# Kernel tuning notes

Hardware: AMD Instinct MI355X
Metric: run time of the kernel (lower is better)

## Reference

```python
import jax, jax.numpy as jnp
import numpy as np

DIM = 320
D_STATE = 32
D_CONV = 4
EXPAND = 2
HEADDIM = 80
D_INNER = EXPAND * DIM          # 640
NHEADS = D_INNER // HEADDIM     # 8
NGROUPS = 1
CONV_DIM = D_INNER + 2 * NGROUPS * D_STATE          # 704
D_IN_PROJ = 2 * D_INNER + 2 * NGROUPS * D_STATE + NHEADS  # 1352
PATCH = (16, 16, 16)
NUM_PT_EMB = 2


def setup_inputs() -> dict:
    key = jax.random.key(0)
    ks = jax.random.split(key, 16)
    B, Np = 4, 8
    x = jax.random.normal(ks[0], (B, DIM) + PATCH, dtype=jnp.float32)
    point_coords = jax.random.uniform(ks[1], (B, Np, 3), dtype=jnp.float32) * jnp.asarray(PATCH, jnp.float32)
    point_labels = jax.random.randint(ks[2], (B, Np), 0, 2)
    return {
        "x": x,
        "point_coords": point_coords,
        "ln_w": jnp.ones((DIM,), jnp.float32),
        "ln_b": jnp.zeros((DIM,), jnp.float32),
        "in_proj_w": jax.random.normal(ks[3], (D_IN_PROJ, DIM), jnp.float32) * 0.02,
        "conv_w": jax.random.normal(ks[4], (CONV_DIM, 1, D_CONV), jnp.float32) * 0.2,
        "conv_b": jax.random.normal(ks[5], (CONV_DIM,), jnp.float32) * 0.02,
        "dt_bias": jax.random.uniform(ks[6], (NHEADS,), jnp.float32, 0.0, 0.1),
        "A_log": jnp.log(jax.random.uniform(ks[7], (NHEADS,), jnp.float32, 1.0, 16.0)),
        "Dp": jnp.ones((NHEADS,), jnp.float32),
        "rms_w": jnp.ones((D_INNER,), jnp.float32),
        "out_proj_w": jax.random.normal(ks[8], (DIM, D_INNER), jnp.float32) * 0.02,
        "pe_gauss": jax.random.normal(ks[9], (3, DIM // 2), jnp.float32),
        "point_embed": jax.random.normal(ks[10], (NUM_PT_EMB, DIM), jnp.float32) * 0.02,
        "not_a_point": jax.random.normal(ks[11], (DIM,), jnp.float32) * 0.02,
        "point_labels": point_labels,
    }


def _forward(x, point_coords, ln_w, ln_b, in_proj_w, conv_w, conv_b, dt_bias,
             A_log, Dp, rms_w, out_proj_w, pe_gauss, point_embed, not_a_point,
             point_labels):
    B, C = x.shape[:2]
    img_dims = x.shape[2:]
    n_tokens = int(np.prod(img_dims))
    xf = x.reshape(B, C, n_tokens).transpose(0, 2, 1)  # (B, T, C)

    # ---- PointEncoder (SAM-style random Fourier positional embedding) ----
    pc = point_coords / jnp.asarray(PATCH, x.dtype)     # normalize to [0,1]
    pc = 2.0 * pc - 1.0
    pe = (2.0 * jnp.pi) * (pc @ pe_gauss)               # (B, Np, DIM/2)
    pemb = jnp.concatenate([jnp.sin(pe), jnp.cos(pe)], axis=-1)  # (B, Np, DIM)
    lbl = point_labels[..., None]
    safe = jnp.clip(point_labels, 0, NUM_PT_EMB - 1)
    pemb = jnp.where(lbl == -1, not_a_point, pemb + point_embed[safe])

    seq = jnp.concatenate([xf, pemb], axis=1)           # (B, L, C)
    L = seq.shape[1]

    # ---- LayerNorm ----
    mu = seq.mean(-1, keepdims=True)
    var = jnp.mean((seq - mu) ** 2, axis=-1, keepdims=True)
    xn = (seq - mu) * jax.lax.rsqrt(var + 1e-5) * ln_w + ln_b

    # ---- Mamba2 ----
    zxbcdt = xn @ in_proj_w.T                            # (B, L, 1352)
    z = zxbcdt[..., :D_INNER]
    xBC = zxbcdt[..., D_INNER:D_INNER + CONV_DIM]
    dt = zxbcdt[..., D_INNER + CONV_DIM:]                # (B, L, H)
    dt = jax.nn.softplus(dt + dt_bias)

    # causal depthwise conv1d over channels
    conv = jax.lax.conv_general_dilated(
        xBC.transpose(0, 2, 1), conv_w, (1,), [(D_CONV - 1, 0)],
        feature_group_count=CONV_DIM,
        dimension_numbers=("NCH", "OIH", "NCH"))
    xBC = jax.nn.silu((conv + conv_b[None, :, None]).transpose(0, 2, 1))

    xs = xBC[..., :D_INNER].reshape(B, L, NHEADS, HEADDIM)
    Bm = xBC[..., D_INNER:D_INNER + D_STATE]             # (B, L, N), ngroups=1
    Cm = xBC[..., D_INNER + D_STATE:]                    # (B, L, N)

    A = -jnp.exp(A_log)                                  # (H,)
    dA = jnp.exp(dt * A)                                 # (B, L, H)

    def step(h, inp):
        dA_t, dt_t, B_t, C_t, x_t = inp
        h = h * dA_t[:, :, None, None] + jnp.einsum('bh,bn,bhp->bhpn', dt_t, B_t, x_t)
        y = jnp.einsum('bhpn,bn->bhp', h, C_t)
        return h, y

    inps = (dA.transpose(1, 0, 2), dt.transpose(1, 0, 2),
            Bm.transpose(1, 0, 2), Cm.transpose(1, 0, 2),
            xs.transpose(1, 0, 2, 3))
    h0 = jnp.zeros((B, NHEADS, HEADDIM, D_STATE), x.dtype)
    _, ys = jax.lax.scan(step, h0, inps)                 # (L, B, H, P)
    y = ys.transpose(1, 0, 2, 3) + xs * Dp[None, None, :, None]
    y = y.reshape(B, L, D_INNER)

    # gated RMSNorm
    y = y * jax.nn.silu(z)
    y = y * jax.lax.rsqrt(jnp.mean(y * y, axis=-1, keepdims=True) + 1e-5) * rms_w
    out = y @ out_proj_w.T                               # (B, L, DIM)

    out = out[:, :n_tokens].transpose(0, 2, 1).reshape(B, C, *img_dims)
    return out


def reference(x, point_coords, ln_w, ln_b, in_proj_w, conv_w, conv_b, dt_bias,
              A_log, Dp, rms_w, out_proj_w, pe_gauss, point_embed, not_a_point,
              point_labels):
    return _forward(x, point_coords, ln_w, ln_b, in_proj_w, conv_w, conv_b,
                    dt_bias, A_log, Dp, rms_w, out_proj_w, pe_gauss,
                    point_embed, not_a_point, point_labels)
```

## Files before the change

### kernel.cpp

```cpp
#include <hip/hip_runtime.h>
#include <math.h>

#define BQ 4
#define LQ 4104
#define NTQ 4096
#define CDIM 320
#define DIP 1352
#define DI 640
#define CONVD 704
#define NH 8
#define HD 80
#define DS 32
#define MQ (BQ*LQ)
#define QC 64
#define NC 65

typedef __attribute__((ext_vector_type(8))) short bf16x8;
typedef __attribute__((ext_vector_type(4))) float f32x4;

__device__ __forceinline__ unsigned short f2bf(float f){
  union { float f; unsigned u; } v; v.f = f;
  unsigned r = v.u + 0x7FFFu + ((v.u >> 16) & 1u);
  return (unsigned short)(r >> 16);
}
__device__ __forceinline__ float bf2f(unsigned short u){
  union { unsigned u; float f; } v; v.u = ((unsigned)u) << 16;
  return v.f;
}
__device__ __forceinline__ float warp_sum(float v){
  #pragma unroll
  for (int o = 32; o; o >>= 1) v += __shfl_xor(v, o);
  return v;
}
__device__ __forceinline__ void gload16(const unsigned short* g, unsigned short* l){
  __builtin_amdgcn_global_load_lds(
      (const __attribute__((address_space(1))) unsigned int*)g,
      (__attribute__((address_space(3))) unsigned int*)l, 16, 0, 0);
}
__device__ __forceinline__ int swz64(int p, int i){
  return p*QC + (i ^ ((p & 7) << 3));
}

__global__ __launch_bounds__(256) void k_prep(
    const float* __restrict__ w1, unsigned short* __restrict__ w1h,
    const float* __restrict__ w2, const float* __restrict__ rsw,
    unsigned short* __restrict__ w2h,
    const float* __restrict__ x, float* __restrict__ muP, float* __restrict__ s2P,
    const float* __restrict__ pcoords, const float* __restrict__ lnw,
    const float* __restrict__ lnb, const float* __restrict__ pgauss,
    const float* __restrict__ pemb_w, const float* __restrict__ nap,
    const int* __restrict__ plabels, unsigned short* __restrict__ xnh)
{
  const int N1 = DIP*CDIM/4;
  const int N2 = CDIM*DI/4;
  const int NBW = (N1 + N2 + 255)/256;
  int bid = blockIdx.x;
  int t = threadIdx.x;

  if (bid < NBW) {
    int i4 = bid*256 + t;
    if (i4 < N1) {
      float4 v = ((const float4*)w1)[i4];
      unsigned short o[4] = {f2bf(v.x), f2bf(v.y), f2bf(v.z), f2bf(v.w)};
      *(uint2*)&w1h[i4*4] = *(const uint2*)o;
    } else if (i4 - N1 < N2) {
      int j = i4 - N1;
      float4 v = ((const float4*)w2)[j];
      float4 wv = *(const float4*)(rsw + (j*4) % DI);
      unsigned short o[4] = {f2bf(v.x*wv.x), f2bf(v.y*wv.y),
                             f2bf(v.z*wv.z), f2bf(v.w*wv.w)};
      *(uint2*)&w2h[j*4] = *(const uint2*)o;
    }
    return;
  }
  bid -= NBW;
  if (bid < 512) {
    int xblk = bid & 15, sl = (bid >> 4) & 7, b = bid >> 7;
    int cs0 = sl * 40;
    int tok = xblk*256 + t;
    const float* xb = x + ((size_t)b*CDIM)*NTQ;
    float s = 0.f, s2 = 0.f;
    #pragma unroll 8
    for (int c = cs0; c < cs0 + 40; c++) {
      float v = xb[(size_t)c*NTQ + tok];
      s += v; s2 = fmaf(v, v, s2);
    }
    muP[((size_t)sl*BQ + b)*NTQ + tok] = s;
    s2P[((size_t)sl*BQ + b)*NTQ + tok] = s2;
    return;
  }
  bid -= 512;
  int j = bid & 7, b = bid >> 3;
  float p0 = pcoords[(b*8+j)*3+0]*(2.0f/16.0f) - 1.0f;
  float p1 = pcoords[(b*8+j)*3+1]*(2.0f/16.0f) - 1.0f;
  float p2 = pcoords[(b*8+j)*3+2]*(2.0f/16.0f) - 1.0f;
  int lab = plabels[b*8+j];
  int safe = lab < 0 ? 0 : (lab > 1 ? 1 : lab);
  float vA, vB = 0.f;
  {
    int cc = t;
    int f = (cc < 160) ? cc : cc - 160;
    float pe = 6.283185307179586f*(p0*pgauss[f] + p1*pgauss[160+f] + p2*pgauss[320+f]);
    float pv = (cc < 160) ? sinf(pe) : cosf(pe);
    vA = (lab == -1) ? nap[cc] : pv + pemb_w[safe*CDIM + cc];
  }
  if (t < 64) {
    int cc = t + 256;
    int f = cc - 160;
    float pe = 6.283185307179586f*(p0*pgauss[f] + p1*pgauss[160+f] + p2*pgauss[320+f]);
    float pv = cosf(pe);
    vB = (lab == -1) ? nap[cc] : pv + pemb_w[safe*CDIM + cc];
  }
  float s  = warp_sum(vA + vB);
  float s2 = warp_sum(vA*vA + vB*vB);
  __shared__ float r1[4], r2[4];
  int w = t >> 6, lane = t & 63;
  if (lane == 0) { r1[w] = s; r2[w] = s2; }
  __syncthreads();
  float ts  = r1[0]+r1[1]+r1[2]+r1[3];
  float ts2 = r2[0]+r2[1]+r2[2]+r2[3];
  float mu   = ts * (1.0f/CDIM);
  float rsig = rsqrtf(ts2*(1.0f/CDIM) - mu*mu + 1e-5f);
  size_t base = ((size_t)b*LQ + NTQ + j)*CDIM;
  xnh[base + t] = f2bf((vA - mu)*rsig*lnw[t] + lnb[t]);
  if (t < 64)
    xnh[base + t + 256] = f2bf((vB - mu)*rsig*lnw[t+256] + lnb[t+256]);
}

__global__ __launch_bounds__(256) void k_norm_t(
    const float* __restrict__ x, const float* __restrict__ muP,
    const float* __restrict__ s2P, const float* __restrict__ lnw,
    const float* __restrict__ lnb, unsigned short* __restrict__ xnh)
{
  int b = blockIdx.z;
  int c0 = blockIdx.y * 64;
  int t0 = blockIdx.x * 64;
  int t = threadIdx.x;
  int lt = t & 63, cg = t >> 6;
  const float* xb = x + ((size_t)b*CDIM)*NTQ;

  __shared__ unsigned short T[64][72];
  __shared__ float muL[64], rsL[64];
  if (t < 64) {
    float s = 0.f, s2 = 0.f;
    #pragma unroll
    for (int sl = 0; sl < 8; sl++) {
      s  += muP[((size_t)sl*BQ + b)*NTQ + t0 + t];
      s2 += s2P[((size_t)sl*BQ + b)*NTQ + t0 + t];
    }
    float mu = s*(1.0f/CDIM);
    muL[t] = mu;
    rsL[t] = rsqrtf(s2*(1.0f/CDIM) - mu*mu + 1e-5f);
  }
  __syncthreads();
  float mu = muL[lt], rs = rsL[lt];
  #pragma unroll
  for (int c = cg; c < 64; c += 4) {
    float v = xb[(size_t)(c0+c)*NTQ + t0 + lt];
    T[lt][c] = f2bf((v - mu)*rs*lnw[c0+c] + lnb[c0+c]);
  }
  __syncthreads();
  #pragma unroll
  for (int i = 0; i < 4; i++) {
    int idx = t + 256*i;
    int tok = idx >> 4, cq = idx & 15;
    *(uint2*)&xnh[((size_t)(b*LQ) + t0 + tok)*CDIM + c0 + cq*4] =
        *(const uint2*)&T[tok][cq*4];
  }
}

__global__ __launch_bounds__(256) void k_gemm1_mfma(
    const unsigned short* __restrict__ Abf, const unsigned short* __restrict__ Wbf,
    unsigned short* __restrict__ zxh, float* __restrict__ dtraw)
{
  __shared__ unsigned short SM[16384];
#define AS1(buf) (SM + (buf)*4096)
#define BS1(buf) (SM + 8192 + (buf)*4096)
  int id = blockIdx.x;
  int xcd = id & 7, pos = id >> 3;
  const int q = 177, r = 3;
  int swz = (xcd < r ? xcd*(q+1) : r*(q+1) + (xcd-r)*q) + pos;
  int m0 = (swz / 11) * 128;
  int n0 = (swz % 11) * 128;
  int tid = threadIdx.x;
  int lane = tid & 63, wid = tid >> 6;
  int wr = wid >> 1, wc = wid & 1;
  int fr = lane & 15, fq = lane >> 4;
  int srow = lane >> 2;
  int scol = (lane & 3) * 8;

#define G1_STAGE(buf, kk)                                                   \
  {                                                                         \
    _Pragma("unroll")                                                       \
    for (int i = 0; i < 2; i++) {                                           \
      int seg = wid + i*4;                                                  \
      int rowA = seg*16 + srow;                                             \
      int ga = m0 + rowA; if (ga > MQ-1) ga = MQ-1;                         \
      gload16(Abf + (size_t)ga*CDIM + (kk) + scol, AS1(buf) + seg*512);     \
      int gb = n0 + rowA; if (gb > DIP-1) gb = DIP-1;                       \
      gload16(Wbf + (size_t)gb*CDIM + (kk) + scol, BS1(buf) + seg*512);     \
    }                                                                       \
  }

#define G1_COMPUTE(buf)                                                     \
  {                                                                         \
    bf16x8 fa[4], fb[4];                                                    \
    _Pragma("unroll")                                                       \
    for (int i = 0; i < 4; i++) {                                           \
      fa[i] = *(const bf16x8*)(AS1(buf) + (wr*64 + i*16 + fr)*32 + fq*8);   \
      fb[i] = *(const bf16x8*)(BS1(buf) + (wc*64 + i*16 + fr)*32 + fq*8);   \
    }                                                                       \
    _Pragma("unroll")                                                       \
    for (int i = 0; i < 4; i++)                                             \
      _Pragma("unroll")                                                     \
      for (int j = 0; j < 4; j++)                                           \
        acc[i][j] = __builtin_amdgcn_mfma_f32_16x16x32_bf16(fa[i], fb[j], acc[i][j], 0, 0, 0); \
  }

  f32x4 acc[4][4] = {};
  G1_STAGE(0, 0);
  __syncthreads();
  int cur = 0;
  for (int k0 = 32; k0 < CDIM; k0 += 32) {
    G1_STAGE(cur^1, k0);
    G1_COMPUTE(cur);
    __syncthreads();
    cur ^= 1;
  }
  G1_COMPUTE(cur);
  __syncthreads();

  #pragma unroll
  for (int i = 0; i < 4; i++) {
    #pragma unroll
    for (int j = 0; j < 4; j++) {
      #pragma unroll
      for (int rr = 0; rr < 4; rr++) {
        int rowL = wr*64 + i*16 + fq*4 + rr;
        int colL = wc*64 + j*16 + fr;
        float v = acc[i][j][rr];
        int gcol = n0 + colL;
        if (gcol >= DI + CONVD && gcol < DIP && m0 + rowL < MQ)
          dtraw[(size_t)(m0+rowL)*NH + (gcol - (DI + CONVD))] = v;
        int g = colL >> 3;
        int gs = (g + 2*fq) & 15;
        SM[rowL*128 + gs*8 + (colL & 7)] = f2bf(v);
      }
    }
  }
  __syncthreads();
  int rows = MQ - m0; if (rows > 128) rows = 128;
  int cols = DIP - n0; if (cols > 128) cols = 128;
  #pragma unroll
  for (int it = 0; it < 8; it++) {
    int idx = tid + it*256;
    int row = idx >> 4, g = idx & 15;
    int fqr = (row >> 2) & 3;
    int gs = (g + 2*fqr) & 15;
    if (row < rows && g*8 < cols)
      *(uint4*)&zxh[(size_t)(m0+row)*DIP + n0 + g*8] = *(const uint4*)&SM[row*128 + gs*8];
  }
}

__global__ __launch_bounds__(256) void k_conv(
    const unsigned short* __restrict__ zxh, const float* __restrict__ cw,
    const float* __restrict__ cb, unsigned short* __restrict__ xcb)
{
  const int nC4 = CONVD/4;
  int gid = blockIdx.x*256 + threadIdx.x;
  if (gid >= (MQ/8)*nC4) return;
  int c4 = gid % nC4;
  int mb = gid / nC4;
  int m0 = mb*8;
  int l0 = m0 % LQ;
  int c0 = c4*4;
  float4 cbv = *(const float4*)(cb + c0);
  float4 w0 = *(const float4*)(cw + (c0+0)*4);
  float4 w1 = *(const float4*)(cw + (c0+1)*4);
  float4 w2 = *(const float4*)(cw + (c0+2)*4);
  float4 w3 = *(const float4*)(cw + (c0+3)*4);
  const float* wp[4] = {(const float*)&w0, (const float*)&w1,
                        (const float*)&w2, (const float*)&w3};
  float vals[11][4];
  #pragma unroll
  for (int r = 0; r < 11; r++) {
    int ls = l0 - 3 + r;
    uint2 u = make_uint2(0,0);
    if (ls >= 0)
      u = *(const uint2*)(zxh + (size_t)(m0-3+r)*DIP + DI + c0);
    vals[r][0] = bf2f((unsigned short)(u.x & 0xffff));
    vals[r][1] = bf2f((unsigned short)(u.x >> 16));
    vals[r][2] = bf2f((unsigned short)(u.y & 0xffff));
    vals[r][3] = bf2f((unsigned short)(u.y >> 16));
  }
  const float* cbp = (const float*)&cbv;
  #pragma unroll
  for (int u = 0; u < 8; u++) {
    unsigned short o[4];
    #pragma unroll
    for (int ch = 0; ch < 4; ch++) {
      float a = cbp[ch];
      #pragma unroll
      for (int j = 0; j < 4; j++)
        a = fmaf(vals[u+j][ch], wp[ch][j], a);
      o[ch] = f2bf(a / (1.f + __expf(-a)));
    }
    *(uint2*)(xcb + (size_t)(m0+u)*CONVD + c0) = *(const uint2*)o;
  }
}

__global__ __launch_bounds__(256) void k_cumsum_state(
    const float* __restrict__ dtraw, const float* __restrict__ dt_bias,
    const float* __restrict__ A_log, const unsigned short* __restrict__ xcb,
    float* __restrict__ dtb, float* __restrict__ cs, float* __restrict__ Dc,
    float* __restrict__ Sbuf)
{
  int c = blockIdx.x, h = blockIdx.y, b = blockIdx.z;
  int len = LQ - c*QC; if (len > QC) len = QC;
  int t = threadIdx.x;
  int lane = t & 63, wid = t >> 6;
  int fr = lane & 15, fq = lane >> 4;
  int m0 = b*LQ + c*QC;

  __shared__ unsigned short XT[HD*QC];
  __shared__ unsigned short BwT[DS*QC];
  __shared__ float ws[QC];

  for (int idx = t; idx < (HD/8)*QC; idx += 256) {
    int pg = idx % 10, i = idx / 10;
    uint4 v = make_uint4(0,0,0,0);
    if (i < len)
      v = *(const uint4*)(xcb + (size_t)(m0+i)*CONVD + h*HD + pg*8);
    union { uint4 u; unsigned short us[8]; } cv; cv.u = v;
    #pragma unroll
    for (int e = 0; e < 8; e++)
      XT[swz64(pg*8+e, i)] = cv.us[e];
  }

  if (t < QC) {
    float A = -expf(A_log[h]);
    float sp = 0.f;
    if (t < len) {
      float v = dtraw[((size_t)(m0+t))*NH + h] + dt_bias[h];
      sp = (v > 20.f) ? v : log1pf(expf(v));
      dtb[((size_t)(m0+t))*NH + h] = sp;
    }
    float a = sp * A;
    #pragma unroll
    for (int off = 1; off < 64; off <<= 1) {
      float pv = __shfl_up(a, off, 64);
      if (t >= off) a += pv;
    }
    cs[((size_t)(b*NH+h)*NC + c)*QC + t] = a;
    if (t == len-1) Dc[(b*NH+h)*NC + c] = expf(a);
    float aEnd = __shfl(a, len-1, 64);
    ws[t] = (t < len) ? __expf(aEnd - a) * sp : 0.f;
  }
  __syncthreads();
  for (int idx = t; idx < DS*QC; idx += 256) {
    int n = idx & 31, i = idx >> 5;
    float v = (i < len) ? bf2f(xcb[(size_t)(m0+i)*CONVD + DI + n]) * ws[i] : 0.f;
    BwT[swz64(n, i)] = f2bf(v);
  }
  __syncthreads();

  size_t base = ((size_t)(b*NC + c)*NH + h)*(HD*DS);
  for (int tp = wid; tp < 10; tp += 4) {
    int pi = tp >> 1, ni = tp & 1;
    f32x4 acc = {};
    #pragma unroll
    for (int ks = 0; ks < 2; ks++) {
      bf16x8 fa = *(const bf16x8*)&XT[swz64(pi*16 + fr, ks*32 + fq*8)];
      bf16x8 fb = *(const bf16x8*)&BwT[swz64(ni*16 + fr, ks*32 + fq*8)];
      acc = __builtin_amdgcn_mfma_f32_16x16x32_bf16(fa, fb, acc, 0, 0, 0);
    }
    #pragma unroll
    for (int rr = 0; rr < 4; rr++)
      Sbuf[base + (size_t)(pi*16 + fq*4 + rr)*DS + ni*16 + fr] = acc[rr];
  }
}

__global__ __launch_bounds__(256) void k_state_scan(
    const float* __restrict__ Sbuf, const float* __restrict__ Dc,
    unsigned short* __restrict__ H0h)
{
  int tid = blockIdx.x*256 + threadIdx.x;
  int pn = tid % (HD*DS);
  int bh = tid / (HD*DS);
  int b = bh >> 3, h = bh & 7;
  float hst = 0.f;
  for (int c = 0; c < NC; c++) {
    size_t idx = ((size_t)(b*NC + c)*NH + h)*(HD*DS) + pn;
    float sv = Sbuf[idx];
    H0h[idx] = f2bf(hst);
    hst = hst * Dc[bh*NC + c] + sv;
  }
}

__global__ __launch_bounds__(256) void k_chunk_y_mfma(
    const unsigned short* __restrict__ xcb, const unsigned short* __restrict__ zxh,
    const float* __restrict__ dtb, const float* __restrict__ cs,
    const unsigned short* __restrict__ H0h, const float* __restrict__ Dp,
    unsigned short* __restrict__ ygb, float* __restrict__ ssum8)
{
  int c = blockIdx.x, h = blockIdx.y, b = blockIdx.z;
  int len = LQ - c*QC; if (len > QC) len = QC;
  int t = threadIdx.x;
  int lane = t & 63, wid = t >> 6;
  int fr = lane & 15, fq = lane >> 4;
  int m0 = b*LQ + c*QC;

  __shared__ unsigned short XT[HD*QC];
  __shared__ unsigned short Wt[4*16*32];
  __shared__ float slA[QC], dtlA[QC], elA[QC];

  const float* csb = cs + ((size_t)(b*NH+h)*NC + c)*QC;

  for (int idx = t; idx < (HD/8)*QC; idx += 256) {
    int pg = idx % 10, i = idx / 10;
    uint4 v = make_uint4(0,0,0,0);
    if (i < len)
      v = *(const uint4*)(xcb + (size_t)(m0+i)*CONVD + h*HD + pg*8);
    union { uint4 u; unsigned short us[8]; } cv; cv.u = v;
    #pragma unroll
    for (int e = 0; e < 8; e++)
      XT[swz64(pg*8+e, i)] = cv.us[e];
  }
  if (t < QC) {
    float s = csb[t];
    slA[t] = s;
    elA[t] = __expf(s);
    dtlA[t] = (t < len) ? dtb[((size_t)(m0+t))*NH + h] : 0.f;
  }
  __syncthreads();

  int row16 = wid*16 + fr;
  bf16x8 fa = {};
  if (row16 < len)
    fa = *(const bf16x8*)(xcb + (size_t)(m0+row16)*CONVD + DI + DS + fq*8);

  size_t hb = ((size_t)(b*NC + c)*NH + h)*(HD*DS);
  f32x4 acc[5];
  #pragma unroll
  for (int j = 0; j < 5; j++) {
    int p = j*16 + fr;
    bf16x8 fb = *(const bf16x8*)(H0h + hb + (size_t)p*DS + fq*8);
    f32x4 z = {};
    acc[j] = __builtin_amdgcn_mfma_f32_16x16x32_bf16(fa, fb, z, 0, 0, 0);
  }
  #pragma unroll
  for (int rr = 0; rr < 4; rr++) {
    float el = elA[wid*16 + fq*4 + rr];
    #pragma unroll
    for (int j = 0; j < 5; j++) acc[j][rr] *= el;
  }

  int wbase = wid << 9;
  for (int sc = 0; sc < 2; sc++) {
    int i0 = sc*32;
    #pragma unroll
    for (int jt = 0; jt < 2; jt++) {
      int col = i0 + jt*16 + fr;
      bf16x8 fbv = {};
      if (col < len)
        fbv = *(const bf16x8*)(xcb + (size_t)(m0+col)*CONVD + DI + fq*8);
      float sc_col = slA[col], dt_col = dtlA[col];
      f32x4 z = {};
      f32x4 g = __builtin_amdgcn_mfma_f32_16x16x32_bf16(fa, fbv, z, 0, 0, 0);
      #pragma unroll
      for (int rr = 0; rr < 4; rr++) {
        int lr = fq*4 + rr;
        int row = wid*16 + lr;
        float v = 0.f;
        if (col <= row)
          v = g[rr] * __expf(slA[row] - sc_col) * dt_col;
        int lc = jt*16 + fr;
        int slot = (lc >> 3) ^ (lr & 3);
        Wt[wbase + (lr<<5) + (slot<<3) + (lc&7)] = f2bf(v);
      }
    }
    bf16x8 wa = *(const bf16x8*)&Wt[wbase + (fr<<5) + ((fq ^ (fr&3))<<3)];
    #pragma unroll
    for (int j = 0; j < 5; j++) {
      int p = j*16 + fr;
      bf16x8 xb = *(const bf16x8*)&XT[swz64(p, i0 + fq*8)];
      acc[j] = __builtin_amdgcn_mfma_f32_16x16x32_bf16(wa, xb, acc[j], 0, 0, 0);
    }
  }

  float dpv = Dp[h];
  #pragma unroll
  for (int rr = 0; rr < 4; rr++) {
    int l = wid*16 + fq*4 + rr;
    if (l >= len) continue;
    size_t m = m0 + l;
    float ssp = 0.f;
    #pragma unroll
    for (int j = 0; j < 5; j++) {
      int p = j*16 + fr;
      int cc = h*HD + p;
      float xv = bf2f(XT[swz64(p, l)]);
      float y = acc[j][rr] + xv*dpv;
      float zv = bf2f(zxh[m*DIP + cc]);
      y *= zv / (1.f + __expf(-zv));
      ygb[m*DI + cc] = f2bf(y);
      ssp = fmaf(y, y, ssp);
    }
    #pragma unroll
    for (int o = 1; o < 16; o <<= 1) ssp += __shfl_xor(ssp, o);
    if (fr == 0) ssum8[m*NH + h] = ssp;
  }
}

__global__ __launch_bounds__(256) void k_gemm2_mfma(
    const unsigned short* __restrict__ W2h, const unsigned short* __restrict__ Ygh,
    const float* __restrict__ ssum8, float* __restrict__ out)
{
  __shared__ unsigned short As[2][128*32];
  __shared__ unsigned short Bs[2][128*32];
  int id = blockIdx.x;
  int xcd = id & 7, pos = id >> 3;
  const int q = 48, r = 3;
  int swz = (xcd < r ? xcd*(q+1) : r*(q+1) + (xcd-r)*q) + pos;
  int c0 = (swz % 3) * 128;
  int t0 = (swz / 3) * 128;
  int tid = threadIdx.x;
  int lane = tid & 63, wid = tid >> 6;
  int wr = wid >> 1, wc = wid & 1;
  int fr = lane & 15, fq = lane >> 4;
  int srow = lane >> 2;
  int scol = (lane & 3) * 8;

#define G2_STAGE(buf, kk)                                                   \
  {                                                                         \
    _Pragma("unroll")                                                       \
    for (int i = 0; i < 2; i++) {                                           \
      int seg = wid + i*4;                                                  \
      int rowA = seg*16 + srow;                                             \
      int ga = c0 + rowA; if (ga > CDIM-1) ga = CDIM-1;                     \
      gload16(W2h + (size_t)ga*DI + (kk) + scol, &As[buf][seg*512]);        \
      int gb = t0 + rowA; if (gb > MQ-1) gb = MQ-1;                         \
      gload16(Ygh + (size_t)gb*DI + (kk) + scol, &Bs[buf][seg*512]);        \
    }                                                                       \
  }

#define G2_COMPUTE(buf)                                                     \
  {                                                                         \
    bf16x8 fa[4], fb[4];                                                    \
    _Pragma("unroll")                                                       \
    for (int i = 0; i < 4; i++) {                                           \
      fa[i] = *(const bf16x8*)&As[buf][(wr*64 + i*16 + fr)*32 + fq*8];      \
      fb[i] = *(const bf16x8*)&Bs[buf][(wc*64 + i*16 + fr)*32 + fq*8];      \
    }                                                                       \
    _Pragma("unroll")                                                       \
    for (int i = 0; i < 4; i++)                                             \
      _Pragma("unroll")                                                     \
      for (int j = 0; j < 4; j++)                                           \
        acc[i][j] = __builtin_amdgcn_mfma_f32_16x16x32_bf16(fa[i], fb[j], acc[i][j], 0, 0, 0); \
  }

  f32x4 acc[4][4] = {};
  G2_STAGE(0, 0);
  __syncthreads();
  int cur = 0;
  for (int k0 = 32; k0 < DI; k0 += 32) {
    G2_STAGE(cur^1, k0);
    G2_COMPUTE(cur);
    __syncthreads();
    cur ^= 1;
  }
  G2_COMPUTE(cur);

  float rsvj[4];
  #pragma unroll
  for (int j = 0; j < 4; j++) {
    int tok = t0 + wc*64 + j*16 + fr;
    float ss = 0.f;
    if (tok < MQ) {
      float4 a = *(const float4*)(ssum8 + (size_t)tok*NH);
      float4 bb = *(const float4*)(ssum8 + (size_t)tok*NH + 4);
      ss = (a.x + a.y + a.z + a.w) + (bb.x + bb.y + bb.z + bb.w);
    }
    rsvj[j] = rsqrtf(ss*(1.0f/DI) + 1e-5f);
  }

  #pragma unroll
  for (int i = 0; i < 4; i++) {
    #pragma unroll
    for (int j = 0; j < 4; j++) {
      #pragma unroll
      for (int rr = 0; rr < 4; rr++) {
        int ch  = c0 + wr*64 + i*16 + fq*4 + rr;
        int tok = t0 + wc*64 + j*16 + fr;
        if (ch < CDIM && tok < MQ) {
          int b = tok / LQ, l = tok % LQ;
          if (l < NTQ)
            out[((size_t)(b*CDIM + ch))*NTQ + l] = acc[i][j][rr] * rsvj[j];
        }
      }
    }
  }
}

extern "C" void kernel_launch(void* const* d_in, const int* in_sizes, int n_in,
                              void* d_out, int out_size, void* d_ws, size_t ws_size,
                              hipStream_t stream)
{
  const float* x       = (const float*)d_in[0];
  const float* pc      = (const float*)d_in[1];
  const float* lnw     = (const float*)d_in[2];
  const float* lnb     = (const float*)d_in[3];
  const float* w1      = (const float*)d_in[4];
  const float* cw      = (const float*)d_in[5];
  const float* cb      = (const float*)d_in[6];
  const float* dt_bias = (const float*)d_in[7];
  const float* A_log   = (const float*)d_in[8];
  const float* Dp      = (const float*)d_in[9];
  const float* rsw     = (const float*)d_in[10];
  const float* w2      = (const float*)d_in[11];
  const float* pg      = (const float*)d_in[12];
  const float* pew     = (const float*)d_in[13];
  const float* nap     = (const float*)d_in[14];
  const int*   plab    = (const int*)d_in[15];
  float* out = (float*)d_out;

  unsigned short* xnh  = (unsigned short*)d_ws;
  unsigned short* zxh  = xnh + (size_t)MQ*CDIM;
  float* dtraw = (float*)(zxh + (size_t)MQ*DIP);
  unsigned short* xcb  = (unsigned short*)(dtraw + (size_t)MQ*NH);
  float* dtb = (float*)(xcb + (size_t)MQ*CONVD);
  float* cs  = dtb + (size_t)MQ*NH;
  float* Dc  = cs  + (size_t)BQ*NH*NC*QC;
  float* Sb  = Dc  + (size_t)BQ*NH*NC;
  unsigned short* H0h = (unsigned short*)(Sb + (size_t)BQ*NC*NH*HD*DS);
  unsigned short* ygb = H0h + (size_t)BQ*NC*NH*HD*DS;
  unsigned short* w1h = ygb + (size_t)MQ*DI;
  unsigned short* w2h = w1h + (size_t)DIP*CDIM;
  float* muP = (float*)(w2h + (size_t)CDIM*DI);
  float* s2P = muP + (size_t)8*BQ*NTQ;
  float* ssum8 = s2P + (size_t)8*BQ*NTQ;

  const int NBW = (DIP*CDIM/4 + CDIM*DI/4 + 255)/256;
  k_prep<<<NBW + 512 + 32, 256, 0, stream>>>(
      w1, w1h, w2, rsw, w2h, x, muP, s2P,
      pc, lnw, lnb, pg, pew, nap, plab, xnh);
  dim3 gn(NTQ/64, CDIM/64, BQ);
  k_norm_t<<<gn, 256, 0, stream>>>(x, muP, s2P, lnw, lnb, xnh);
  k_gemm1_mfma<<<129*11, 256, 0, stream>>>(xnh, w1h, zxh, dtraw);
  k_conv<<<((MQ/8)*(CONVD/4) + 255)/256, 256, 0, stream>>>(zxh, cw, cb, xcb);
  dim3 gc(NC, NH, BQ);
  k_cumsum_state<<<gc, 256, 0, stream>>>(dtraw, dt_bias, A_log, xcb, dtb, cs, Dc, Sb);
  k_state_scan<<<(BQ*NH*HD*DS)/256, 256, 0, stream>>>(Sb, Dc, H0h);
  k_chunk_y_mfma<<<gc, 256, 0, stream>>>(xcb, zxh, dtb, cs, H0h, Dp, ygb, ssum8);
  k_gemm2_mfma<<<129*3, 256, 0, stream>>>(w2h, ygb, ssum8, out);
}
```

Measured before the change: 145.2 us.

## Fuse LayerNorm statistics and normalization into one single-pass kernel

Removes the partial mean/variance pass from the prep kernel and the separate normalize-transpose kernel. It replaces them with one kernel that loads all 320 channels for 32 tokens into shared memory, reduces statistics there, and writes normalized bf16 rows. This avoids reading x twice and the muP/s2P round trip through global memory. In exchange it uses about 42KB of shared memory per block, which may lower occupancy, and it launches only 512 blocks.

```diff
diff --git a/kernel.cpp b/kernel.cpp
--- a/kernel.cpp
+++ b/kernel.cpp
@@ -45,7 +45,6 @@
     const float* __restrict__ w1, unsigned short* __restrict__ w1h,
     const float* __restrict__ w2, const float* __restrict__ rsw,
     unsigned short* __restrict__ w2h,
-    const float* __restrict__ x, float* __restrict__ muP, float* __restrict__ s2P,
     const float* __restrict__ pcoords, const float* __restrict__ lnw,
     const float* __restrict__ lnb, const float* __restrict__ pgauss,
     const float* __restrict__ pemb_w, const float* __restrict__ nap,
@@ -74,22 +73,6 @@
     return;
   }
   bid -= NBW;
-  if (bid < 512) {
-    int xblk = bid & 15, sl = (bid >> 4) & 7, b = bid >> 7;
-    int cs0 = sl * 40;
-    int tok = xblk*256 + t;
-    const float* xb = x + ((size_t)b*CDIM)*NTQ;
-    float s = 0.f, s2 = 0.f;
-    #pragma unroll 8
-    for (int c = cs0; c < cs0 + 40; c++) {
-      float v = xb[(size_t)c*NTQ + tok];
-      s += v; s2 = fmaf(v, v, s2);
-    }
-    muP[((size_t)sl*BQ + b)*NTQ + tok] = s;
-    s2P[((size_t)sl*BQ + b)*NTQ + tok] = s2;
-    return;
-  }
-  bid -= 512;
   int j = bid & 7, b = bid >> 3;
   float p0 = pcoords[(b*8+j)*3+0]*(2.0f/16.0f) - 1.0f;
   float p1 = pcoords[(b*8+j)*3+1]*(2.0f/16.0f) - 1.0f;
@@ -127,45 +110,51 @@
     xnh[base + t + 256] = f2bf((vB - mu)*rsig*lnw[t+256] + lnb[t+256]);
 }
 
-__global__ __launch_bounds__(256) void k_norm_t(
-    const float* __restrict__ x, const float* __restrict__ muP,
-    const float* __restrict__ s2P, const float* __restrict__ lnw,
+__global__ __launch_bounds__(256) void k_ln(
+    const float* __restrict__ x, const float* __restrict__ lnw,
     const float* __restrict__ lnb, unsigned short* __restrict__ xnh)
 {
-  int b = blockIdx.z;
-  int c0 = blockIdx.y * 64;
-  int t0 = blockIdx.x * 64;
+  int b = blockIdx.y;
+  int t0 = blockIdx.x * 32;
   int t = threadIdx.x;
-  int lt = t & 63, cg = t >> 6;
+  int lt = t & 31, cg = t >> 5;
   const float* xb = x + ((size_t)b*CDIM)*NTQ;
 
-  __shared__ unsigned short T[64][72];
-  __shared__ float muL[64], rsL[64];
-  if (t < 64) {
-    float s = 0.f, s2 = 0.f;
-    #pragma unroll
-    for (int sl = 0; sl < 8; sl++) {
-      s  += muP[((size_t)sl*BQ + b)*NTQ + t0 + t];
-      s2 += s2P[((size_t)sl*BQ + b)*NTQ + t0 + t];
-    }
-    float mu = s*(1.0f/CDIM);
+  __shared__ float XC[CDIM][33];
+  __shared__ float sA[8][32], s2A[8][32];
+  __shared__ float muL[32], rsL[32];
+
+  float s = 0.f, s2 = 0.f;
+  for (int c = cg; c < CDIM; c += 8) {
+    float v = xb[(size_t)c*NTQ + t0 + lt];
+    s += v; s2 = fmaf(v, v, s2);
+    XC[c][lt] = v;
+  }
+  sA[cg][lt] = s; s2A[cg][lt] = s2;
+  __syncthreads();
+  if (t < 32) {
+    float ts = 0.f, ts2 = 0.f;
+    #pragma unroll
+    for (int g = 0; g < 8; g++) { ts += sA[g][t]; ts2 += s2A[g][t]; }
+    float mu = ts*(1.0f/CDIM);
     muL[t] = mu;
-    rsL[t] = rsqrtf(s2*(1.0f/CDIM) - mu*mu + 1e-5f);
-  }
-  __syncthreads();
-  float mu = muL[lt], rs = rsL[lt];
-  #pragma unroll
-  for (int c = cg; c < 64; c += 4) {
-    float v = xb[(size_t)(c0+c)*NTQ + t0 + lt];
-    T[lt][c] = f2bf((v - mu)*rs*lnw[c0+c] + lnb[c0+c]);
-  }
-  __syncthreads();
-  #pragma unroll
-  for (int i = 0; i < 4; i++) {
-    int idx = t + 256*i;
-    int tok = idx >> 4, cq = idx & 15;
-    *(uint2*)&xnh[((size_t)(b*LQ) + t0 + tok)*CDIM + c0 + cq*4] =
-        *(const uint2*)&T[tok][cq*4];
+    rsL[t] = rsqrtf(ts2*(1.0f/CDIM) - mu*mu + 1e-5f);
+  }
+  __syncthreads();
+  #pragma unroll
+  for (int it = 0; it < 10; it++) {
+    int idx = t + it*256;
+    int tok = idx / 80, g4 = idx % 80;
+    int c0 = g4*4;
+    float mu = muL[tok], rs = rsL[tok];
+    float4 wv = *(const float4*)(lnw + c0);
+    float4 bv = *(const float4*)(lnb + c0);
+    unsigned short o[4];
+    o[0] = f2bf((XC[c0+0][tok] - mu)*rs*wv.x + bv.x);
+    o[1] = f2bf((XC[c0+1][tok] - mu)*rs*wv.y + bv.y);
+    o[2] = f2bf((XC[c0+2][tok] - mu)*rs*wv.z + bv.z);
+    o[3] = f2bf((XC[c0+3][tok] - mu)*rs*wv.w + bv.w);
+    *(uint2*)&xnh[((size_t)(b*LQ) + t0 + tok)*CDIM + c0] = *(const uint2*)o;
   }
 }
 
@@ -636,16 +625,14 @@
   unsigned short* ygb = H0h + (size_t)BQ*NC*NH*HD*DS;
   unsigned short* w1h = ygb + (size_t)MQ*DI;
   unsigned short* w2h = w1h + (size_t)DIP*CDIM;
-  float* muP = (float*)(w2h + (size_t)CDIM*DI);
-  float* s2P = muP + (size_t)8*BQ*NTQ;
-  float* ssum8 = s2P + (size_t)8*BQ*NTQ;
+  float* ssum8 = (float*)(w2h + (size_t)CDIM*DI);
 
   const int NBW = (DIP*CDIM/4 + CDIM*DI/4 + 255)/256;
-  k_prep<<<NBW + 512 + 32, 256, 0, stream>>>(
-      w1, w1h, w2, rsw, w2h, x, muP, s2P,
+  k_prep<<<NBW + 32, 256, 0, stream>>>(
+      w1, w1h, w2, rsw, w2h,
       pc, lnw, lnb, pg, pew, nap, plab, xnh);
-  dim3 gn(NTQ/64, CDIM/64, BQ);
-  k_norm_t<<<gn, 256, 0, stream>>>(x, muP, s2P, lnw, lnb, xnh);
+  dim3 gl(NTQ/32, BQ);
+  k_ln<<<gl, 256, 0, stream>>>(x, lnw, lnb, xnh);
   k_gemm1_mfma<<<129*11, 256, 0, stream>>>(xnh, w1h, zxh, dtraw);
   k_conv<<<((MQ/8)*(CONVD/4) + 255)/256, 256, 0, stream>>>(zxh, cw, cb, xcb);
   dim3 gc(NC, NH, BQ);
```

Measured after the change: 154.9 us. 1.07x slower.
